# Kernel optimization log

Measured on AMD Instinct MI355X. Metric: run time of the kernel, lower is better.

## Reference

```python
import jax, jax.numpy as jnp
import numpy as np

H, C, HID, L, NF, B = 4, 128, 128, 3, 5, 32  # heads, per-head dim, hidden, layers, node feats, graphs
LN_EPS = 1e-5


def setup_inputs() -> dict:
    key = jax.random.key(0)
    ks = jax.random.split(key, 12)
    N, E = 10000, 160000
    x = jax.random.normal(ks[0], (N, NF), dtype=jnp.float32)
    edge_index = jax.random.randint(ks[1], (2, E), 0, N, dtype=jnp.int64)
    batch = jnp.sort(jax.random.randint(ks[2], (N,), 0, B, dtype=jnp.int64))
    s = 0.1
    return {
        "x": x,
        "edge_index": edge_index,
        "batch": batch,
        "node_W": jax.random.normal(ks[3], (NF, HID), dtype=jnp.float32) * s,
        "node_b": jnp.zeros((HID,), dtype=jnp.float32),
        "Ws": jax.random.normal(ks[4], (L, HID, H * C), dtype=jnp.float32) * s,
        "att_srcs": jax.random.normal(ks[5], (L, H, C), dtype=jnp.float32) * s,
        "att_dsts": jax.random.normal(ks[6], (L, H, C), dtype=jnp.float32) * s,
        "biases": jnp.zeros((L, HID), dtype=jnp.float32),
        "ln_gs": jnp.ones((L, HID), dtype=jnp.float32),
        "ln_bs": jnp.zeros((L, HID), dtype=jnp.float32),
    }


def _layer_norm(x, g, b):
    mu = jnp.mean(x, axis=-1, keepdims=True)
    var = jnp.mean(jnp.square(x - mu), axis=-1, keepdims=True)
    return (x - mu) * jax.lax.rsqrt(var + LN_EPS) * g + b


def _gat_layer(x, W, att_src, att_dst, bias, src, dst, N):
    # x: [N, HID]; PyG GATConv, heads=H, concat=False (mean over heads)
    h = (x @ W).reshape(N, H, C)                       # [N,H,C]
    a_src = jnp.sum(h * att_src, axis=-1)              # [N,H]
    a_dst = jnp.sum(h * att_dst, axis=-1)              # [N,H]
    e = jax.nn.leaky_relu(a_src[src] + a_dst[dst], 0.2)  # [E,H]
    # edge-softmax over destination neighborhoods (numerically stable)
    m = jax.ops.segment_max(e, dst, num_segments=N)
    ex = jnp.exp(e - m[dst])
    denom = jax.ops.segment_sum(ex, dst, num_segments=N)
    alpha = ex / (denom[dst] + 1e-16)                  # [E,H]
    msg = h[src] * alpha[:, :, None]                   # [E,H,C]
    out = jax.ops.segment_sum(msg, dst, num_segments=N)  # [N,H,C]
    return out.mean(axis=1) + bias                     # concat=False -> head mean


def reference(x, edge_index, batch, node_W, node_b, Ws, att_srcs, att_dsts,
              biases, ln_gs, ln_bs):
    N = x.shape[0]
    loop = jnp.arange(N, dtype=edge_index.dtype)
    src = jnp.concatenate([edge_index[0], loop])       # PyG adds self-loops
    dst = jnp.concatenate([edge_index[1], loop])

    h = jax.nn.relu(x @ node_W + node_b)               # [N,HID]
    for l in range(L):
        h_new = _gat_layer(h, Ws[l], att_srcs[l], att_dsts[l], biases[l], src, dst, N)
        h_new = _layer_norm(h_new, ln_gs[l], ln_bs[l])
        h = jax.nn.relu(h_new) + h                     # residual; dropout is identity in eval

    # global mean pool over graphs
    sums = jax.ops.segment_sum(h, batch, num_segments=B)
    cnts = jax.ops.segment_sum(jnp.ones((N, 1), h.dtype), batch, num_segments=B)
    graph_emb = sums / jnp.maximum(cnts, 1.0)
    return h, graph_emb
```

## Files before the change

kernel.cpp:

```cpp
#include <hip/hip_runtime.h>
#include <math.h>

#define N_NODES 10000
#define N_EDGES 160000
#define E2 (N_EDGES + N_NODES)
#define HIDDEN 128
#define NHEAD 4
#define NB 32
#define LN_EPS 1e-5f

__device__ __forceinline__ unsigned short f2bf(float f) {
    unsigned int u = __float_as_uint(f);
    u += 0x7fffu + ((u >> 16) & 1u);
    return (unsigned short)(u >> 16);
}
__device__ __forceinline__ float bf2f_lo(unsigned int u) { return __uint_as_float(u << 16); }
__device__ __forceinline__ float bf2f_hi(unsigned int u) { return __uint_as_float(u & 0xffff0000u); }

__global__ void k_init(int* counts, int* gstart, int* gend, float* gout) {
    int i = blockIdx.x * blockDim.x + threadIdx.x;
    if (i < N_NODES) counts[i] = 1;
    if (i < NB) { gstart[i] = N_NODES; gend[i] = 0; }
    if (i < NB * HIDDEN) gout[i] = 0.f;
}

__global__ void k_hist(const int* __restrict__ ei, int* counts) {
    int e = blockIdx.x * blockDim.x + threadIdx.x;
    if (e < N_EDGES) atomicAdd(&counts[ei[N_EDGES + e]], 1);
}

__global__ void k_scan(const int* __restrict__ counts, int* rowptr, int* cursor) {
    __shared__ int sums[1024];
    int t = threadIdx.x;
    const int per = 10;
    int base = t * per;
    int loc[per];
    int s = 0;
    for (int i = 0; i < per; i++) {
        int idx = base + i;
        int v = (idx < N_NODES) ? counts[idx] : 0;
        loc[i] = s; s += v;
    }
    sums[t] = s;
    __syncthreads();
    for (int off = 1; off < 1024; off <<= 1) {
        int v = (t >= off) ? sums[t - off] : 0;
        __syncthreads();
        sums[t] += v;
        __syncthreads();
    }
    int prefix = (t > 0) ? sums[t - 1] : 0;
    for (int i = 0; i < per; i++) {
        int idx = base + i;
        if (idx < N_NODES) { int r = prefix + loc[i]; rowptr[idx] = r; cursor[idx] = r; }
    }
    if (t == 1023) rowptr[N_NODES] = sums[1023];
}

__global__ void k_scatter(const int* __restrict__ ei, int* cursor, int* csr_src) {
    int e = blockIdx.x * blockDim.x + threadIdx.x;
    if (e < N_EDGES) {
        int s = ei[e], d = ei[N_EDGES + e];
        int pos = atomicAdd(&cursor[d], 1);
        csr_src[pos] = s;
    } else if (e < E2) {
        int n = e - N_EDGES;
        int pos = atomicAdd(&cursor[n], 1);
        csr_src[pos] = n;
    }
}

__global__ void k_bounds(const int* __restrict__ batch, int* gstart, int* gend) {
    int n = blockIdx.x * blockDim.x + threadIdx.x;
    if (n >= N_NODES) return;
    int b = batch[n];
    if (n == 0 || batch[n - 1] != b) gstart[b] = n;
    if (n == N_NODES - 1 || batch[n + 1] != b) gend[b] = n + 1;
}

__global__ void k_input(const float* __restrict__ x, const float* __restrict__ W,
                        const float* __restrict__ b, float* __restrict__ h) {
    int t = blockIdx.x * blockDim.x + threadIdx.x;
    if (t >= N_NODES * HIDDEN) return;
    int n = t >> 7, c = t & 127;
    float s = b[c];
    #pragma unroll
    for (int k = 0; k < 5; k++) s += x[n * 5 + k] * W[k * HIDDEN + c];
    h[t] = fmaxf(s, 0.f);
}

#define BM 64
#define BN 64
#define BK 32
__global__ __launch_bounds__(256) void k_gemm(const float* __restrict__ A,
                                              const float* __restrict__ Bw,
                                              unsigned short* __restrict__ Cb) {
    __shared__ float As[BK][BM + 1];
    __shared__ float Bs[BK][BN];
    int tid = threadIdx.x;
    int tx = tid & 15, ty = tid >> 4;
    int mbase = blockIdx.y * BM;
    int nbase = blockIdx.x * BN;
    float acc[4][4] = {};
    for (int k0 = 0; k0 < HIDDEN; k0 += BK) {
        #pragma unroll
        for (int r = 0; r < 2; r++) {
            int idx = tid + r * 256;
            int row = idx >> 3;
            int k4 = (idx & 7) << 2;
            int grow = mbase + row;
            float4 v = make_float4(0.f, 0.f, 0.f, 0.f);
            if (grow < N_NODES) v = *(const float4*)(A + (size_t)grow * HIDDEN + k0 + k4);
            As[k4 + 0][row] = v.x; As[k4 + 1][row] = v.y;
            As[k4 + 2][row] = v.z; As[k4 + 3][row] = v.w;
        }
        #pragma unroll
        for (int r = 0; r < 2; r++) {
            int idx = tid + r * 256;
            int row = idx >> 4;
            int c4 = (idx & 15) << 2;
            *(float4*)(&Bs[row][c4]) = *(const float4*)(Bw + (size_t)(k0 + row) * 512 + nbase + c4);
        }
        __syncthreads();
        #pragma unroll
        for (int k = 0; k < BK; k++) {
            float a0 = As[k][ty * 4 + 0], a1 = As[k][ty * 4 + 1];
            float a2 = As[k][ty * 4 + 2], a3 = As[k][ty * 4 + 3];
            float b0 = Bs[k][tx * 4 + 0], b1 = Bs[k][tx * 4 + 1];
            float b2 = Bs[k][tx * 4 + 2], b3 = Bs[k][tx * 4 + 3];
            acc[0][0] += a0 * b0; acc[0][1] += a0 * b1; acc[0][2] += a0 * b2; acc[0][3] += a0 * b3;
            acc[1][0] += a1 * b0; acc[1][1] += a1 * b1; acc[1][2] += a1 * b2; acc[1][3] += a1 * b3;
            acc[2][0] += a2 * b0; acc[2][1] += a2 * b1; acc[2][2] += a2 * b2; acc[2][3] += a2 * b3;
            acc[3][0] += a3 * b0; acc[3][1] += a3 * b1; acc[3][2] += a3 * b2; acc[3][3] += a3 * b3;
        }
        __syncthreads();
    }
    #pragma unroll
    for (int i = 0; i < 4; i++) {
        int gr = mbase + ty * 4 + i;
        if (gr < N_NODES) {
            ushort4 v;
            v.x = f2bf(acc[i][0]); v.y = f2bf(acc[i][1]);
            v.z = f2bf(acc[i][2]); v.w = f2bf(acc[i][3]);
            *(ushort4*)(Cb + (size_t)gr * 512 + nbase + tx * 4) = v;
        }
    }
}

__global__ void k_att(const unsigned int* __restrict__ hb32,
                      const float* __restrict__ ws,
                      const float* __restrict__ wd, float* __restrict__ a_src,
                      float* __restrict__ a_dst) {
    int widx = blockIdx.x * 4 + (threadIdx.x >> 6);
    int lane = threadIdx.x & 63;
    if (widx >= N_NODES * NHEAD) return;
    int n = widx >> 2, h = widx & 3;
    unsigned int u = hb32[(size_t)n * 256 + h * 64 + lane];
    float v0 = bf2f_lo(u), v1 = bf2f_hi(u);
    int c = 2 * lane;
    float s = v0 * ws[h * 128 + c] + v1 * ws[h * 128 + c + 1];
    float d = v0 * wd[h * 128 + c] + v1 * wd[h * 128 + c + 1];
    #pragma unroll
    for (int o = 32; o > 0; o >>= 1) { s += __shfl_down(s, o); d += __shfl_down(d, o); }
    if (lane == 0) { a_src[widx] = s; a_dst[widx] = d; }
}

__global__ __launch_bounds__(256) void k_agg(const uint4* __restrict__ hb4,
                                             const int* __restrict__ rowptr,
                                             const int* __restrict__ csr,
                                             const float* __restrict__ a_src,
                                             const float* __restrict__ a_dst,
                                             const float* __restrict__ bias,
                                             const float* __restrict__ lng,
                                             const float* __restrict__ lnb,
                                             float* __restrict__ h) {
    int wave = threadIdx.x >> 6;
    int lane = threadIdx.x & 63;
    int n = blockIdx.x * 4 + wave;
    if (n >= N_NODES) return;
    int hl = lane >> 4;
    int pos = lane & 15;
    int off = rowptr[n];
    int deg = rowptr[n + 1] - off;
    float adn = a_dst[n * 4 + hl];
    float m = -INFINITY, denom = 0.f;
    float o[8] = {};
    for (int base = 0; base < deg; base += 64) {
        int cnt = min(64, deg - base);
        int s = (lane < cnt) ? csr[off + base + lane] : 0;
        for (int i = 0; i < cnt; i++) {
            int si = __shfl(s, i);
            float t = a_src[si * 4 + hl] + adn;
            float e = t > 0.f ? t : 0.2f * t;
            float nm = fmaxf(m, e);
            float sc = __expf(m - nm);
            float p = __expf(e - nm);
            denom = denom * sc + p;
            uint4 u = hb4[(size_t)si * 64 + lane];
            o[0] = o[0] * sc + p * bf2f_lo(u.x);
            o[1] = o[1] * sc + p * bf2f_hi(u.x);
            o[2] = o[2] * sc + p * bf2f_lo(u.y);
            o[3] = o[3] * sc + p * bf2f_hi(u.y);
            o[4] = o[4] * sc + p * bf2f_lo(u.z);
            o[5] = o[5] * sc + p * bf2f_hi(u.z);
            o[6] = o[6] * sc + p * bf2f_lo(u.w);
            o[7] = o[7] * sc + p * bf2f_hi(u.w);
            m = nm;
        }
    }
    float inv = 1.f / (denom + 1e-16f);
    #pragma unroll
    for (int k = 0; k < 8; k++) o[k] *= inv;
    #pragma unroll
    for (int k = 0; k < 8; k++) {
        o[k] += __shfl_xor(o[k], 16);
        o[k] += __shfl_xor(o[k], 32);
    }
    float v[8], sv = 0.f, sq = 0.f;
    #pragma unroll
    for (int k = 0; k < 8; k++) {
        float b = bias[8 * pos + k];
        v[k] = 0.25f * o[k] + b;
        sv += v[k]; sq += v[k] * v[k];
    }
    #pragma unroll
    for (int d = 8; d > 0; d >>= 1) {
        sv += __shfl_xor(sv, d);
        sq += __shfl_xor(sq, d);
    }
    float mu = sv * (1.f / 128.f);
    float var = sq * (1.f / 128.f) - mu * mu;
    float rs = rsqrtf(var + LN_EPS);
    if (hl == 0) {
        float* hrow = h + (size_t)n * 128 + 8 * pos;
        float4 old0 = *(const float4*)(hrow);
        float4 old1 = *(const float4*)(hrow + 4);
        float r[8];
        #pragma unroll
        for (int k = 0; k < 8; k++) {
            float y = (v[k] - mu) * rs * lng[8 * pos + k] + lnb[8 * pos + k];
            r[k] = fmaxf(y, 0.f);
        }
        float4 w0 = make_float4(r[0] + old0.x, r[1] + old0.y, r[2] + old0.z, r[3] + old0.w);
        float4 w1 = make_float4(r[4] + old1.x, r[5] + old1.y, r[6] + old1.z, r[7] + old1.w);
        *(float4*)(hrow) = w0;
        *(float4*)(hrow + 4) = w1;
    }
}

#define POOL_CHUNK 32
__global__ __launch_bounds__(128) void k_pool_sum(const float* __restrict__ h,
                                                  const int* __restrict__ batch,
                                                  float* __restrict__ gout) {
    int n0 = blockIdx.x * POOL_CHUNK;
    int c = threadIdx.x;
    int nend = min(n0 + POOL_CHUNK, N_NODES);
    if (n0 >= N_NODES) return;
    int cur = batch[n0];
    float acc = 0.f;
    for (int n = n0; n < nend; n++) {
        int b = batch[n];
        if (b != cur) {
            atomicAdd(&gout[cur * HIDDEN + c], acc);
            acc = 0.f; cur = b;
        }
        acc += h[(size_t)n * HIDDEN + c];
    }
    atomicAdd(&gout[cur * HIDDEN + c], acc);
}

__global__ void k_pool_div(const int* __restrict__ gstart, const int* __restrict__ gend,
                           float* __restrict__ gout) {
    int b = blockIdx.x, c = threadIdx.x;
    int cnt = gend[b] - gstart[b];
    gout[b * HIDDEN + c] *= 1.f / (float)max(cnt, 1);
}

extern "C" void kernel_launch(void* const* d_in, const int* in_sizes, int n_in,
                              void* d_out, int out_size, void* d_ws, size_t ws_size,
                              hipStream_t stream) {
    const float* x      = (const float*)d_in[0];
    const int*   ei     = (const int*)d_in[1];
    const int*   batch  = (const int*)d_in[2];
    const float* node_W = (const float*)d_in[3];
    const float* node_b = (const float*)d_in[4];
    const float* Ws     = (const float*)d_in[5];
    const float* att_s  = (const float*)d_in[6];
    const float* att_d  = (const float*)d_in[7];
    const float* biases = (const float*)d_in[8];
    const float* ln_g   = (const float*)d_in[9];
    const float* ln_b   = (const float*)d_in[10];

    float* out = (float*)d_out;
    float* h = out;
    float* gout = out + (size_t)N_NODES * HIDDEN;

    char* w = (char*)d_ws;
    auto carve = [&](size_t bytes) {
        void* p = (void*)w;
        w += (bytes + 255) & ~(size_t)255;
        return p;
    };
    int* rowptr  = (int*)carve((N_NODES + 1) * sizeof(int));
    int* cursor  = (int*)carve(N_NODES * sizeof(int));
    int* counts  = (int*)carve(N_NODES * sizeof(int));
    int* csr     = (int*)carve(E2 * sizeof(int));
    int* gstart  = (int*)carve(NB * sizeof(int));
    int* gend    = (int*)carve(NB * sizeof(int));
    float* a_src = (float*)carve((size_t)N_NODES * NHEAD * sizeof(float));
    float* a_dst = (float*)carve((size_t)N_NODES * NHEAD * sizeof(float));
    unsigned short* hb = (unsigned short*)carve((size_t)N_NODES * 512 * sizeof(unsigned short));

    k_init<<<(N_NODES + 255) / 256, 256, 0, stream>>>(counts, gstart, gend, gout);
    k_hist<<<(N_EDGES + 255) / 256, 256, 0, stream>>>(ei, counts);
    k_scan<<<1, 1024, 0, stream>>>(counts, rowptr, cursor);
    k_scatter<<<(E2 + 255) / 256, 256, 0, stream>>>(ei, cursor, csr);
    k_bounds<<<(N_NODES + 255) / 256, 256, 0, stream>>>(batch, gstart, gend);
    k_input<<<(N_NODES * HIDDEN + 255) / 256, 256, 0, stream>>>(x, node_W, node_b, h);

    for (int l = 0; l < 3; l++) {
        k_gemm<<<dim3(512 / BN, (N_NODES + BM - 1) / BM), 256, 0, stream>>>(
            h, Ws + (size_t)l * HIDDEN * 512, hb);
        k_att<<<N_NODES, 256, 0, stream>>>((const unsigned int*)hb,
                                           att_s + l * NHEAD * 128,
                                           att_d + l * NHEAD * 128, a_src, a_dst);
        k_agg<<<(N_NODES + 3) / 4, 256, 0, stream>>>((const uint4*)hb, rowptr, csr,
                                           a_src, a_dst,
                                           biases + l * HIDDEN, ln_g + l * HIDDEN,
                                           ln_b + l * HIDDEN, h);
    }
    k_pool_sum<<<(N_NODES + POOL_CHUNK - 1) / POOL_CHUNK, 128, 0, stream>>>(h, batch, gout);
    k_pool_div<<<NB, HIDDEN, 0, stream>>>(gstart, gend, gout);
}
```

Baseline: 303.2 us.

## Use bf16 MFMA for projection GEMM with bf16 activation copies

Replaces the fp32 shared-memory SIMT GEMM with a bf16 MFMA 16x16x32 kernel that loads operands directly from global memory. The layer weights are pre-transposed and converted to bf16 once, and the input and aggregation kernels now also write a bf16 copy of the node features for the next GEMM. This removes fp32 FMA work and shared-memory traffic, at the cost of lower-precision GEMM inputs, an extra bf16 store per layer, and scattered 2-byte output stores.

```diff
diff --git a/kernel.cpp b/kernel.cpp
--- a/kernel.cpp
+++ b/kernel.cpp
@@ -8,6 +8,9 @@
 #define NHEAD 4
 #define NB 32
 #define LN_EPS 1e-5f
+
+typedef __attribute__((ext_vector_type(8))) short bf16x8;
+typedef __attribute__((ext_vector_type(4))) float f32x4;
 
 __device__ __forceinline__ unsigned short f2bf(float f) {
     unsigned int u = __float_as_uint(f);
@@ -78,71 +81,60 @@
     if (n == N_NODES - 1 || batch[n + 1] != b) gend[b] = n + 1;
 }
 
+__global__ void k_convB(const float* __restrict__ Ws, unsigned short* __restrict__ Btb) {
+    int t = blockIdx.x * blockDim.x + threadIdx.x;
+    if (t >= 3 * 512 * 128) return;
+    int l = t >> 16, rem = t & 65535;
+    int n = rem >> 7, k = rem & 127;
+    Btb[t] = f2bf(Ws[l * 65536 + k * 512 + n]);
+}
+
 __global__ void k_input(const float* __restrict__ x, const float* __restrict__ W,
-                        const float* __restrict__ b, float* __restrict__ h) {
+                        const float* __restrict__ b, float* __restrict__ h,
+                        unsigned short* __restrict__ hb) {
     int t = blockIdx.x * blockDim.x + threadIdx.x;
     if (t >= N_NODES * HIDDEN) return;
     int n = t >> 7, c = t & 127;
     float s = b[c];
     #pragma unroll
     for (int k = 0; k < 5; k++) s += x[n * 5 + k] * W[k * HIDDEN + c];
-    h[t] = fmaxf(s, 0.f);
-}
-
-#define BM 64
-#define BN 64
-#define BK 32
-__global__ __launch_bounds__(256) void k_gemm(const float* __restrict__ A,
-                                              const float* __restrict__ Bw,
+    float r = fmaxf(s, 0.f);
+    h[t] = r;
+    hb[t] = f2bf(r);
+}
+
+__global__ __launch_bounds__(256) void k_gemm(const unsigned short* __restrict__ Ab,
+                                              const unsigned short* __restrict__ Bt,
                                               unsigned short* __restrict__ Cb) {
-    __shared__ float As[BK][BM + 1];
-    __shared__ float Bs[BK][BN];
-    int tid = threadIdx.x;
-    int tx = tid & 15, ty = tid >> 4;
-    int mbase = blockIdx.y * BM;
-    int nbase = blockIdx.x * BN;
-    float acc[4][4] = {};
-    for (int k0 = 0; k0 < HIDDEN; k0 += BK) {
+    int wave = threadIdx.x >> 6, lane = threadIdx.x & 63;
+    int q = lane >> 4, u = lane & 15;
+    int mbase = blockIdx.y * 64 + wave * 16;
+    int nbase = blockIdx.x * 64;
+    int arow = mbase + u;
+    if (arow > N_NODES - 1) arow = N_NODES - 1;
+    bf16x8 a[4];
+    #pragma unroll
+    for (int k0 = 0; k0 < 4; k0++)
+        a[k0] = *(const bf16x8*)(Ab + (size_t)arow * 128 + k0 * 32 + q * 8);
+    f32x4 acc[4];
+    #pragma unroll
+    for (int nb = 0; nb < 4; nb++) acc[nb] = (f32x4){0.f, 0.f, 0.f, 0.f};
+    #pragma unroll
+    for (int nb = 0; nb < 4; nb++) {
+        const unsigned short* bp = Bt + (size_t)(nbase + nb * 16 + u) * 128 + q * 8;
         #pragma unroll
-        for (int r = 0; r < 2; r++) {
-            int idx = tid + r * 256;
-            int row = idx >> 3;
-            int k4 = (idx & 7) << 2;
-            int grow = mbase + row;
-            float4 v = make_float4(0.f, 0.f, 0.f, 0.f);
-            if (grow < N_NODES) v = *(const float4*)(A + (size_t)grow * HIDDEN + k0 + k4);
-            As[k4 + 0][row] = v.x; As[k4 + 1][row] = v.y;
-            As[k4 + 2][row] = v.z; As[k4 + 3][row] = v.w;
-        }
+        for (int k0 = 0; k0 < 4; k0++) {
+            bf16x8 bfr = *(const bf16x8*)(bp + k0 * 32);
+            acc[nb] = __builtin_amdgcn_mfma_f32_16x16x32_bf16(a[k0], bfr, acc[nb], 0, 0, 0);
+        }
+    }
+    #pragma unroll
+    for (int nb = 0; nb < 4; nb++) {
+        int col = nbase + nb * 16 + u;
         #pragma unroll
-        for (int r = 0; r < 2; r++) {
-            int idx = tid + r * 256;
-            int row = idx >> 4;
-            int c4 = (idx & 15) << 2;
-            *(float4*)(&Bs[row][c4]) = *(const float4*)(Bw + (size_t)(k0 + row) * 512 + nbase + c4);
-        }
-        __syncthreads();
-        #pragma unroll
-        for (int k = 0; k < BK; k++) {
-            float a0 = As[k][ty * 4 + 0], a1 = As[k][ty * 4 + 1];
-            float a2 = As[k][ty * 4 + 2], a3 = As[k][ty * 4 + 3];
-            float b0 = Bs[k][tx * 4 + 0], b1 = Bs[k][tx * 4 + 1];
-            float b2 = Bs[k][tx * 4 + 2], b3 = Bs[k][tx * 4 + 3];
-            acc[0][0] += a0 * b0; acc[0][1] += a0 * b1; acc[0][2] += a0 * b2; acc[0][3] += a0 * b3;
-            acc[1][0] += a1 * b0; acc[1][1] += a1 * b1; acc[1][2] += a1 * b2; acc[1][3] += a1 * b3;
-            acc[2][0] += a2 * b0; acc[2][1] += a2 * b1; acc[2][2] += a2 * b2; acc[2][3] += a2 * b3;
-            acc[3][0] += a3 * b0; acc[3][1] += a3 * b1; acc[3][2] += a3 * b2; acc[3][3] += a3 * b3;
-        }
-        __syncthreads();
-    }
-    #pragma unroll
-    for (int i = 0; i < 4; i++) {
-        int gr = mbase + ty * 4 + i;
-        if (gr < N_NODES) {
-            ushort4 v;
-            v.x = f2bf(acc[i][0]); v.y = f2bf(acc[i][1]);
-            v.z = f2bf(acc[i][2]); v.w = f2bf(acc[i][3]);
-            *(ushort4*)(Cb + (size_t)gr * 512 + nbase + tx * 4) = v;
+        for (int r = 0; r < 4; r++) {
+            int row = mbase + q * 4 + r;
+            if (row < N_NODES) Cb[(size_t)row * 512 + col] = f2bf(acc[nb][r]);
         }
     }
 }
@@ -173,7 +165,8 @@
                                              const float* __restrict__ bias,
                                              const float* __restrict__ lng,
                                              const float* __restrict__ lnb,
-                                             float* __restrict__ h) {
+                                             float* __restrict__ h,
+                                             unsigned short* __restrict__ hbn) {
     int wave = threadIdx.x >> 6;
     int lane = threadIdx.x & 63;
     int n = blockIdx.x * 4 + wave;
@@ -241,10 +234,16 @@
             float y = (v[k] - mu) * rs * lng[8 * pos + k] + lnb[8 * pos + k];
             r[k] = fmaxf(y, 0.f);
         }
-        float4 w0 = make_float4(r[0] + old0.x, r[1] + old0.y, r[2] + old0.z, r[3] + old0.w);
-        float4 w1 = make_float4(r[4] + old1.x, r[5] + old1.y, r[6] + old1.z, r[7] + old1.w);
-        *(float4*)(hrow) = w0;
-        *(float4*)(hrow + 4) = w1;
+        float w[8] = {r[0] + old0.x, r[1] + old0.y, r[2] + old0.z, r[3] + old0.w,
+                      r[4] + old1.x, r[5] + old1.y, r[6] + old1.z, r[7] + old1.w};
+        *(float4*)(hrow) = make_float4(w[0], w[1], w[2], w[3]);
+        *(float4*)(hrow + 4) = make_float4(w[4], w[5], w[6], w[7]);
+        ushort4 p0, p1;
+        p0.x = f2bf(w[0]); p0.y = f2bf(w[1]); p0.z = f2bf(w[2]); p0.w = f2bf(w[3]);
+        p1.x = f2bf(w[4]); p1.y = f2bf(w[5]); p1.z = f2bf(w[6]); p1.w = f2bf(w[7]);
+        unsigned short* hbrow = hbn + (size_t)n * 128 + 8 * pos;
+        *(ushort4*)(hbrow) = p0;
+        *(ushort4*)(hbrow + 4) = p1;
     }
 }
 
@@ -309,25 +308,28 @@
     int* gend    = (int*)carve(NB * sizeof(int));
     float* a_src = (float*)carve((size_t)N_NODES * NHEAD * sizeof(float));
     float* a_dst = (float*)carve((size_t)N_NODES * NHEAD * sizeof(float));
-    unsigned short* hb = (unsigned short*)carve((size_t)N_NODES * 512 * sizeof(unsigned short));
+    unsigned short* hb  = (unsigned short*)carve((size_t)N_NODES * 512 * sizeof(unsigned short));
+    unsigned short* hbx = (unsigned short*)carve((size_t)N_NODES * HIDDEN * sizeof(unsigned short));
+    unsigned short* Btb = (unsigned short*)carve((size_t)3 * 512 * 128 * sizeof(unsigned short));
 
     k_init<<<(N_NODES + 255) / 256, 256, 0, stream>>>(counts, gstart, gend, gout);
     k_hist<<<(N_EDGES + 255) / 256, 256, 0, stream>>>(ei, counts);
     k_scan<<<1, 1024, 0, stream>>>(counts, rowptr, cursor);
     k_scatter<<<(E2 + 255) / 256, 256, 0, stream>>>(ei, cursor, csr);
     k_bounds<<<(N_NODES + 255) / 256, 256, 0, stream>>>(batch, gstart, gend);
-    k_input<<<(N_NODES * HIDDEN + 255) / 256, 256, 0, stream>>>(x, node_W, node_b, h);
+    k_convB<<<(3 * 512 * 128 + 255) / 256, 256, 0, stream>>>(Ws, Btb);
+    k_input<<<(N_NODES * HIDDEN + 255) / 256, 256, 0, stream>>>(x, node_W, node_b, h, hbx);
 
     for (int l = 0; l < 3; l++) {
-        k_gemm<<<dim3(512 / BN, (N_NODES + BM - 1) / BM), 256, 0, stream>>>(
-            h, Ws + (size_t)l * HIDDEN * 512, hb);
+        k_gemm<<<dim3(8, (N_NODES + 63) / 64), 256, 0, stream>>>(
+            hbx, Btb + (size_t)l * 512 * 128, hb);
         k_att<<<N_NODES, 256, 0, stream>>>((const unsigned int*)hb,
                                            att_s + l * NHEAD * 128,
                                            att_d + l * NHEAD * 128, a_src, a_dst);
         k_agg<<<(N_NODES + 3) / 4, 256, 0, stream>>>((const uint4*)hb, rowptr, csr,
                                            a_src, a_dst,
                                            biases + l * HIDDEN, ln_g + l * HIDDEN,
-                                           ln_b + l * HIDDEN, h);
+                                           ln_b + l * HIDDEN, h, hbx);
     }
     k_pool_sum<<<(N_NODES + POOL_CHUNK - 1) / POOL_CHUNK, 128, 0, stream>>>(h, batch, gout);
     k_pool_div<<<NB, HIDDEN, 0, stream>>>(gstart, gend, gout);
```

After: 290.3 us. -4.2%, faster.
